# Performance work log

Measured on AMD Instinct MI355X. Metric: run time of the kernel, lower is better.

The kernel has to match this reference:

```python
import jax, jax.numpy as jnp
import numpy as np

N_NODES = 200000  # num_users + num_items
N_EDGES = 500000
LATENT = 64
N_LAYERS = 3
NEG_SLOPE = 0.01  # F.leaky_relu default
EPS = 1e-16       # PyG geo_softmax denominator epsilon


def setup_inputs() -> dict:
    key = jax.random.key(0)
    k1, k2, k3, k4, k5 = jax.random.split(key, 5)
    edge_index = jax.random.randint(k1, (2, N_EDGES), 0, N_NODES, dtype=jnp.int64 if jax.config.jax_enable_x64 else jnp.int32)
    edge_attrs = jax.random.normal(k2, (N_EDGES, 2), dtype=jnp.float32)
    emb = jax.random.normal(k3, (N_NODES, LATENT), dtype=jnp.float32)
    # per-layer attention params, shape [L, heads=1 -> squeezed, in_channels]
    a_att_w = jax.random.normal(k4, (N_LAYERS, LATENT), dtype=jnp.float32) * 0.1
    r_att_w = jax.random.normal(k5, (N_LAYERS, LATENT), dtype=jnp.float32) * 0.1
    return {"edge_index": edge_index, "edge_attrs": edge_attrs, "emb": emb,
            "a_att_w": a_att_w, "r_att_w": r_att_w}


def _segment_softmax(scores, dst, num_nodes):
    # scores: [E, D] softmax over edges grouped by destination node (PyG geo_softmax)
    m = jax.ops.segment_max(scores, dst, num_segments=num_nodes)  # [N, D]
    m = jnp.where(jnp.isfinite(m), m, 0.0)  # nodes without incoming edges
    w = jnp.exp(scores - m[dst])
    den = jax.ops.segment_sum(w, dst, num_segments=num_nodes)     # [N, D]
    return w / (den[dst] + EPS)


def reference(edge_index, edge_attrs, emb, a_att_w, r_att_w):
    src, dst = edge_index[0], edge_index[1]
    n = emb.shape[0]
    # symmetric degree normalization (degree of destination endpoints)
    deg = jax.ops.segment_sum(jnp.ones_like(dst, dtype=emb.dtype), dst, num_segments=n)
    dinv = jnp.where(deg > 0, deg ** -0.5, 0.0)
    norm = (dinv[src] * dinv[dst])[:, None]  # [E, 1]

    a_e = edge_attrs[:, 0:1]  # [E, 1]
    r_e = edge_attrs[:, 1:2]

    x = emb
    acc = emb  # layer-0 embedding
    for l in range(N_LAYERS):
        scores = (jax.nn.leaky_relu(a_e * a_att_w[l], NEG_SLOPE)
                  + jax.nn.leaky_relu(r_e * r_att_w[l], NEG_SLOPE))  # [E, D]
        attn = _segment_softmax(scores, dst, n)                       # [E, D]
        msg = norm * attn * x[src]                                    # gather + weight
        x = jax.ops.segment_sum(msg, dst, num_segments=n)             # scatter-add
        acc = acc + x
    out = acc / (N_LAYERS + 1)  # mean over layer embeddings
    return out
```

## Files before the change

kernel.cpp:

```cpp
#include <hip/hip_runtime.h>

#define BLK 256
#define LBLK 256
#define CH 1024

__device__ __forceinline__ unsigned short f2bf(float f) {
    unsigned u = __float_as_uint(f);
    u += 0x7FFFu + ((u >> 16) & 1u);
    return (unsigned short)(u >> 16);
}
__device__ __forceinline__ float bf2f(unsigned short h) {
    return __uint_as_float((unsigned)h << 16);
}
__device__ __forceinline__ float4 unpack4(ushort4 h) {
    return make_float4(bf2f(h.x), bf2f(h.y), bf2f(h.z), bf2f(h.w));
}
__device__ __forceinline__ ushort4 pack4(float4 f) {
    ushort4 h; h.x = f2bf(f.x); h.y = f2bf(f.y); h.z = f2bf(f.z); h.w = f2bf(f.w);
    return h;
}


__global__ void k_deg(const int* __restrict__ dst, int* __restrict__ deg,
                      int* __restrict__ rank, int E) {
    int e = blockIdx.x * blockDim.x + threadIdx.x;
    if (e < E) rank[e] = atomicAdd(&deg[dst[e]], 1);
}

__global__ void k_scan1(const int* __restrict__ deg, int* __restrict__ partials, int N) {
    __shared__ int sm[BLK];
    int i0 = blockIdx.x * CH + threadIdx.x * 4;
    int s = 0;
    if (i0 + 3 < N) {
        int4 v = *(const int4*)(deg + i0);
        s = (v.x + v.y) + (v.z + v.w);
    } else {
        for (int k = 0; k < 4; ++k) if (i0 + k < N) s += deg[i0 + k];
    }
    sm[threadIdx.x] = s;
    __syncthreads();
    for (int off = BLK / 2; off > 0; off >>= 1) {
        if (threadIdx.x < off) sm[threadIdx.x] += sm[threadIdx.x + off];
        __syncthreads();
    }
    if (threadIdx.x == 0) partials[blockIdx.x] = sm[0];
}

__global__ void k_scan2(const int* __restrict__ deg, const int* __restrict__ partials,
                        int* __restrict__ row_off, int N, int E, int nb) {
    __shared__ int sp[BLK];
    __shared__ int sm[BLK];
    int b = blockIdx.x, t = threadIdx.x;
    sp[t] = (t < nb) ? partials[t] : 0;
    __syncthreads();
    for (int off = 1; off < BLK; off <<= 1) {
        int add = (t >= off) ? sp[t - off] : 0;
        __syncthreads();
        sp[t] += add;
        __syncthreads();
    }
    int base = (b == 0) ? 0 : sp[b - 1];
    if (b == 0 && t == 0) row_off[N] = E;
    int i0 = b * CH + t * 4;
    int v0 = 0, v1 = 0, v2 = 0, v3 = 0;
    if (i0 + 3 < N) {
        int4 v = *(const int4*)(deg + i0);
        v0 = v.x; v1 = v.y; v2 = v.z; v3 = v.w;
    } else {
        if (i0     < N) v0 = deg[i0];
        if (i0 + 1 < N) v1 = deg[i0 + 1];
        if (i0 + 2 < N) v2 = deg[i0 + 2];
    }
    int tot = (v0 + v1) + (v2 + v3);
    sm[t] = tot;
    __syncthreads();
    for (int off = 1; off < BLK; off <<= 1) {
        int add = (t >= off) ? sm[t - off] : 0;
        __syncthreads();
        sm[t] += add;
        __syncthreads();
    }
    int excl = base + sm[t] - tot;
    int4 r;
    r.x = excl;
    r.y = excl + v0;
    r.z = excl + v0 + v1;
    r.w = excl + v0 + v1 + v2;
    if (i0 + 3 < N) {
        *(int4*)(row_off + i0) = r;
    } else {
        if (i0     < N) row_off[i0]     = r.x;
        if (i0 + 1 < N) row_off[i0 + 1] = r.y;
        if (i0 + 2 < N) row_off[i0 + 2] = r.z;
    }
}

__global__ void k_convfill(const int* __restrict__ src, const int* __restrict__ dst,
                           const float2* __restrict__ attrs, const int* __restrict__ row_off,
                           const int* __restrict__ rank, const int* __restrict__ deg,
                           uint2* __restrict__ csr, const float4* __restrict__ emb4,
                           ushort4* __restrict__ embs, int E, int N16, int gF) {
    int b = blockIdx.x;
    if (b < gF) {
        int e = b * BLK + threadIdx.x;
        if (e >= E) return;
        int pos = row_off[dst[e]] + rank[e];
        float2 ar = attrs[e];
        csr[pos] = make_uint2((unsigned)src[e],
                              (unsigned)f2bf(ar.x) | ((unsigned)f2bf(ar.y) << 16));
    } else {
        int i = (b - gF) * BLK + threadIdx.x;
        if (i >= N16) return;
        int d = deg[i >> 4];
        float dinv = (d > 0) ? rsqrtf((float)d) : 0.0f;
        float4 e = emb4[i];
        embs[i] = pack4(make_float4(dinv * e.x, dinv * e.y, dinv * e.z, dinv * e.w));
    }
}


__device__ __forceinline__ float lrelu(float x) { return fmaxf(x, 0.01f * x); }

__device__ __forceinline__ float4 edge_w4(unsigned ar, const float4& aw, const float4& rw) {
    float a = bf2f((unsigned short)(ar & 0xffffu));
    float r = bf2f((unsigned short)(ar >> 16));
    float4 w;
    w.x = __expf(lrelu(a * aw.x) + lrelu(r * rw.x));
    w.y = __expf(lrelu(a * aw.y) + lrelu(r * rw.y));
    w.z = __expf(lrelu(a * aw.z) + lrelu(r * rw.z));
    w.w = __expf(lrelu(a * aw.w) + lrelu(r * rw.w));
    return w;
}

__device__ __forceinline__ void acc4(float4& num, float4& den,
                                     const float4& w, const ushort4& h, float g) {
    float4 x = unpack4(h);
    den.x += g * w.x; den.y += g * w.y; den.z += g * w.z; den.w += g * w.w;
    num.x += g * w.x * x.x;
    num.y += g * w.y * x.y;
    num.z += g * w.z * x.z;
    num.w += g * w.w * x.w;
}

template<int MODE>
__global__ __launch_bounds__(LBLK) void k_layer(
    const ushort4* __restrict__ xs, const uint2* __restrict__ csr,
    const int* __restrict__ row_off,
    const float4* __restrict__ aw4, const float4* __restrict__ rw4,
    const float4* __restrict__ emb4,
    const ushort4* __restrict__ xsA, const ushort4* __restrict__ xsB,
    ushort4* __restrict__ xsout, float4* __restrict__ out4, int N) {
    const int t = threadIdx.x;
    const int d4 = t & 15;
    const int v = blockIdx.x * (LBLK / 16) + (t >> 4);
    if (v >= N) return;
    const float4 aw = aw4[d4];
    const float4 rw = rw4[d4];
    const int s0 = row_off[v];
    const int s1 = row_off[v + 1];
    const int dv = s1 - s0;
    float4 num = {0.f, 0.f, 0.f, 0.f};
    float4 den = {0.f, 0.f, 0.f, 0.f};
    for (int i = s0; i < s1; i += 4) {
        const int last = s1 - 1;
        uint2 e0 = csr[i];
        uint2 e1 = csr[min(i + 1, last)];
        uint2 e2 = csr[min(i + 2, last)];
        uint2 e3 = csr[min(i + 3, last)];
        ushort4 h0 = xs[(size_t)e0.x * 16 + d4];
        ushort4 h1 = xs[(size_t)e1.x * 16 + d4];
        ushort4 h2 = xs[(size_t)e2.x * 16 + d4];
        ushort4 h3 = xs[(size_t)e3.x * 16 + d4];
        float4 w0 = edge_w4(e0.y, aw, rw);
        float4 w1 = edge_w4(e1.y, aw, rw);
        float4 w2 = edge_w4(e2.y, aw, rw);
        float4 w3 = edge_w4(e3.y, aw, rw);
        float g1 = (i + 1 < s1) ? 1.0f : 0.0f;
        float g2 = (i + 2 < s1) ? 1.0f : 0.0f;
        float g3 = (i + 3 < s1) ? 1.0f : 0.0f;
        acc4(num, den, w0, h0, 1.0f);
        acc4(num, den, w1, h1, g1);
        acc4(num, den, w2, h2, g2);
        acc4(num, den, w3, h3, g3);
    }
    float4 xr;
    xr.x = num.x / (den.x + 1e-16f);
    xr.y = num.y / (den.y + 1e-16f);
    xr.z = num.z / (den.z + 1e-16f);
    xr.w = num.w / (den.w + 1e-16f);
    const float dinv = (dv > 0) ? rsqrtf((float)dv) : 0.0f;
    const size_t o = (size_t)v * 16 + d4;
    if (MODE == 2) {
        const float sd = (dv > 0) ? sqrtf((float)dv) : 0.0f;
        float4 e = emb4[o];
        float4 A = unpack4(xsA[o]);
        float4 B = unpack4(xsB[o]);
        float4 r;
        r.x = (e.x + sd * (A.x + B.x) + dinv * xr.x) * 0.25f;
        r.y = (e.y + sd * (A.y + B.y) + dinv * xr.y) * 0.25f;
        r.z = (e.z + sd * (A.z + B.z) + dinv * xr.z) * 0.25f;
        r.w = (e.w + sd * (A.w + B.w) + dinv * xr.w) * 0.25f;
        out4[o] = r;
    } else {
        const float s = dinv * dinv;
        xsout[o] = pack4(make_float4(s * xr.x, s * xr.y, s * xr.z, s * xr.w));
    }
}


extern "C" void kernel_launch(void* const* d_in, const int* in_sizes, int n_in,
                              void* d_out, int out_size, void* d_ws, size_t ws_size,
                              hipStream_t stream) {
    const int*   ei    = (const int*)d_in[0];
    const float* attrs = (const float*)d_in[1];
    const float* emb   = (const float*)d_in[2];
    const float* a_att = (const float*)d_in[3];
    const float* r_att = (const float*)d_in[4];

    const int E = in_sizes[0] / 2;
    const int N = in_sizes[2] / 64;
    const int* src = ei;
    const int* dst = ei + E;

    char* ws = (char*)d_ws;
    size_t off = 0;
    auto alloc = [&](size_t bytes) {
        void* p = ws + off;
        off += (bytes + 255) & ~(size_t)255;
        return p;
    };
    int*     deg      = (int*)alloc((size_t)N * 4);
    int*     rank     = (int*)alloc((size_t)E * 4);
    int*     row_off  = (int*)alloc((size_t)(N + 1) * 4);
    int*     partials = (int*)alloc((size_t)BLK * 4);
    uint2*   csr      = (uint2*)alloc((size_t)E * 8);
    ushort4* embs     = (ushort4*)alloc((size_t)N * 16 * 8);
    ushort4* xsA      = (ushort4*)alloc((size_t)N * 16 * 8);
    ushort4* xsB      = (ushort4*)alloc((size_t)N * 16 * 8);
    float4*  out      = (float4*)d_out;

    hipMemsetAsync(deg, 0, (size_t)N * 4, stream);

    int gE = (E + BLK - 1) / BLK;
    int nb = (N + CH - 1) / CH;
    int gF = gE;
    int gC = (N * 16 + BLK - 1) / BLK;

    k_deg     <<<gE, BLK, 0, stream>>>(dst, deg, rank, E);
    k_scan1   <<<nb, BLK, 0, stream>>>(deg, partials, N);
    k_scan2   <<<nb, BLK, 0, stream>>>(deg, partials, row_off, N, E, nb);
    k_convfill<<<gF + gC, BLK, 0, stream>>>(src, dst, (const float2*)attrs, row_off,
                                            rank, deg, csr, (const float4*)emb,
                                            embs, E, N * 16, gF);

    const float4* emb4 = (const float4*)emb;
    const float4* aw4  = (const float4*)a_att;
    const float4* rw4  = (const float4*)r_att;

    int gL = (N + (LBLK / 16) - 1) / (LBLK / 16);
    k_layer<0><<<gL, LBLK, 0, stream>>>(embs, csr, row_off, aw4,      rw4,
                                        nullptr, nullptr, nullptr, xsA, nullptr, N);
    k_layer<1><<<gL, LBLK, 0, stream>>>(xsA,  csr, row_off, aw4 + 16, rw4 + 16,
                                        nullptr, nullptr, nullptr, xsB, nullptr, N);
    k_layer<2><<<gL, LBLK, 0, stream>>>(xsB,  csr, row_off, aw4 + 32, rw4 + 32,
                                        emb4, xsA, xsB, nullptr, out, N);
}
```

Before: 242.2 us.

## Fuse two-pass scan into one kernel with inter-block flags; use exp2 weights

Replaces the two scan kernels with one. Each block publishes its flagged partial sum with a release store, then spin-waits on all earlier partials through acquire loads before computing its prefix. This removes one kernel launch and its dependency gap, but it only works if all 196 blocks run at the same time. Separately, the edge-weight exponent uses exp2f with the attention weights pre-scaled by log2(e), and tail edges are masked by a large negative bias inside the exponent instead of multiplying by a gate.

```diff
diff --git a/kernel.cpp b/kernel.cpp
--- a/kernel.cpp
+++ b/kernel.cpp
@@ -3,6 +3,8 @@
 #define BLK 256
 #define LBLK 256
 #define CH 1024
+#define LOG2E 1.44269504f
+#define SFLAG 0x40000000
 
 __device__ __forceinline__ unsigned short f2bf(float f) {
     unsigned u = __float_as_uint(f);
@@ -27,40 +29,11 @@
     if (e < E) rank[e] = atomicAdd(&deg[dst[e]], 1);
 }
 
-__global__ void k_scan1(const int* __restrict__ deg, int* __restrict__ partials, int N) {
+__global__ void k_scan(const int* __restrict__ deg, int* __restrict__ sync,
+                       int* __restrict__ row_off, int N, int E, int nb) {
     __shared__ int sm[BLK];
-    int i0 = blockIdx.x * CH + threadIdx.x * 4;
-    int s = 0;
-    if (i0 + 3 < N) {
-        int4 v = *(const int4*)(deg + i0);
-        s = (v.x + v.y) + (v.z + v.w);
-    } else {
-        for (int k = 0; k < 4; ++k) if (i0 + k < N) s += deg[i0 + k];
-    }
-    sm[threadIdx.x] = s;
-    __syncthreads();
-    for (int off = BLK / 2; off > 0; off >>= 1) {
-        if (threadIdx.x < off) sm[threadIdx.x] += sm[threadIdx.x + off];
-        __syncthreads();
-    }
-    if (threadIdx.x == 0) partials[blockIdx.x] = sm[0];
-}
-
-__global__ void k_scan2(const int* __restrict__ deg, const int* __restrict__ partials,
-                        int* __restrict__ row_off, int N, int E, int nb) {
     __shared__ int sp[BLK];
-    __shared__ int sm[BLK];
     int b = blockIdx.x, t = threadIdx.x;
-    sp[t] = (t < nb) ? partials[t] : 0;
-    __syncthreads();
-    for (int off = 1; off < BLK; off <<= 1) {
-        int add = (t >= off) ? sp[t - off] : 0;
-        __syncthreads();
-        sp[t] += add;
-        __syncthreads();
-    }
-    int base = (b == 0) ? 0 : sp[b - 1];
-    if (b == 0 && t == 0) row_off[N] = E;
     int i0 = b * CH + t * 4;
     int v0 = 0, v1 = 0, v2 = 0, v3 = 0;
     if (i0 + 3 < N) {
@@ -80,6 +53,25 @@
         sm[t] += add;
         __syncthreads();
     }
+    if (t == 0)
+        __hip_atomic_store(&sync[b], sm[BLK - 1] | SFLAG,
+                           __ATOMIC_RELEASE, __HIP_MEMORY_SCOPE_AGENT);
+    int pv = 0;
+    if (t < nb) {
+        while ((pv = __hip_atomic_load(&sync[t], __ATOMIC_ACQUIRE,
+                                       __HIP_MEMORY_SCOPE_AGENT)) == 0) {}
+        pv &= ~SFLAG;
+    }
+    sp[t] = pv;
+    __syncthreads();
+    for (int off = 1; off < BLK; off <<= 1) {
+        int add = (t >= off) ? sp[t - off] : 0;
+        __syncthreads();
+        sp[t] += add;
+        __syncthreads();
+    }
+    int base = (b == 0) ? 0 : sp[b - 1];
+    if (b == 0 && t == 0) row_off[N] = E;
     int excl = base + sm[t] - tot;
     int4 r;
     r.x = excl;
@@ -121,25 +113,26 @@
 
 __device__ __forceinline__ float lrelu(float x) { return fmaxf(x, 0.01f * x); }
 
-__device__ __forceinline__ float4 edge_w4(unsigned ar, const float4& aw, const float4& rw) {
+__device__ __forceinline__ float4 edge_w4(unsigned ar, const float4& aw, const float4& rw,
+                                          float gb) {
     float a = bf2f((unsigned short)(ar & 0xffffu));
     float r = bf2f((unsigned short)(ar >> 16));
     float4 w;
-    w.x = __expf(lrelu(a * aw.x) + lrelu(r * rw.x));
-    w.y = __expf(lrelu(a * aw.y) + lrelu(r * rw.y));
-    w.z = __expf(lrelu(a * aw.z) + lrelu(r * rw.z));
-    w.w = __expf(lrelu(a * aw.w) + lrelu(r * rw.w));
+    w.x = exp2f(lrelu(a * aw.x) + lrelu(r * rw.x) + gb);
+    w.y = exp2f(lrelu(a * aw.y) + lrelu(r * rw.y) + gb);
+    w.z = exp2f(lrelu(a * aw.z) + lrelu(r * rw.z) + gb);
+    w.w = exp2f(lrelu(a * aw.w) + lrelu(r * rw.w) + gb);
     return w;
 }
 
 __device__ __forceinline__ void acc4(float4& num, float4& den,
-                                     const float4& w, const ushort4& h, float g) {
+                                     const float4& w, const ushort4& h) {
     float4 x = unpack4(h);
-    den.x += g * w.x; den.y += g * w.y; den.z += g * w.z; den.w += g * w.w;
-    num.x += g * w.x * x.x;
-    num.y += g * w.y * x.y;
-    num.z += g * w.z * x.z;
-    num.w += g * w.w * x.w;
+    den.x += w.x; den.y += w.y; den.z += w.z; den.w += w.w;
+    num.x += w.x * x.x;
+    num.y += w.y * x.y;
+    num.z += w.z * x.z;
+    num.w += w.w * x.w;
 }
 
 template<int MODE>
@@ -154,8 +147,10 @@
     const int d4 = t & 15;
     const int v = blockIdx.x * (LBLK / 16) + (t >> 4);
     if (v >= N) return;
-    const float4 aw = aw4[d4];
-    const float4 rw = rw4[d4];
+    float4 aw = aw4[d4];
+    float4 rw = rw4[d4];
+    aw.x *= LOG2E; aw.y *= LOG2E; aw.z *= LOG2E; aw.w *= LOG2E;
+    rw.x *= LOG2E; rw.y *= LOG2E; rw.z *= LOG2E; rw.w *= LOG2E;
     const int s0 = row_off[v];
     const int s1 = row_off[v + 1];
     const int dv = s1 - s0;
@@ -171,17 +166,17 @@
         ushort4 h1 = xs[(size_t)e1.x * 16 + d4];
         ushort4 h2 = xs[(size_t)e2.x * 16 + d4];
         ushort4 h3 = xs[(size_t)e3.x * 16 + d4];
-        float4 w0 = edge_w4(e0.y, aw, rw);
-        float4 w1 = edge_w4(e1.y, aw, rw);
-        float4 w2 = edge_w4(e2.y, aw, rw);
-        float4 w3 = edge_w4(e3.y, aw, rw);
-        float g1 = (i + 1 < s1) ? 1.0f : 0.0f;
-        float g2 = (i + 2 < s1) ? 1.0f : 0.0f;
-        float g3 = (i + 3 < s1) ? 1.0f : 0.0f;
-        acc4(num, den, w0, h0, 1.0f);
-        acc4(num, den, w1, h1, g1);
-        acc4(num, den, w2, h2, g2);
-        acc4(num, den, w3, h3, g3);
+        float gb1 = (i + 1 < s1) ? 0.0f : -1e4f;
+        float gb2 = (i + 2 < s1) ? 0.0f : -1e4f;
+        float gb3 = (i + 3 < s1) ? 0.0f : -1e4f;
+        float4 w0 = edge_w4(e0.y, aw, rw, 0.0f);
+        float4 w1 = edge_w4(e1.y, aw, rw, gb1);
+        float4 w2 = edge_w4(e2.y, aw, rw, gb2);
+        float4 w3 = edge_w4(e3.y, aw, rw, gb3);
+        acc4(num, den, w0, h0);
+        acc4(num, den, w1, h1);
+        acc4(num, den, w2, h2);
+        acc4(num, den, w3, h3);
     }
     float4 xr;
     xr.x = num.x / (den.x + 1e-16f);
@@ -230,16 +225,16 @@
         return p;
     };
     int*     deg      = (int*)alloc((size_t)N * 4);
+    int*     sync     = (int*)alloc((size_t)BLK * 4);
     int*     rank     = (int*)alloc((size_t)E * 4);
     int*     row_off  = (int*)alloc((size_t)(N + 1) * 4);
-    int*     partials = (int*)alloc((size_t)BLK * 4);
     uint2*   csr      = (uint2*)alloc((size_t)E * 8);
     ushort4* embs     = (ushort4*)alloc((size_t)N * 16 * 8);
     ushort4* xsA      = (ushort4*)alloc((size_t)N * 16 * 8);
     ushort4* xsB      = (ushort4*)alloc((size_t)N * 16 * 8);
     float4*  out      = (float4*)d_out;
 
-    hipMemsetAsync(deg, 0, (size_t)N * 4, stream);
+    hipMemsetAsync(deg, 0, (size_t)N * 4 + (size_t)BLK * 4, stream);
 
     int gE = (E + BLK - 1) / BLK;
     int nb = (N + CH - 1) / CH;
@@ -247,8 +242,7 @@
     int gC = (N * 16 + BLK - 1) / BLK;
 
     k_deg     <<<gE, BLK, 0, stream>>>(dst, deg, rank, E);
-    k_scan1   <<<nb, BLK, 0, stream>>>(deg, partials, N);
-    k_scan2   <<<nb, BLK, 0, stream>>>(deg, partials, row_off, N, E, nb);
+    k_scan    <<<nb, BLK, 0, stream>>>(deg, sync, row_off, N, E, nb);
     k_convfill<<<gF + gC, BLK, 0, stream>>>(src, dst, (const float2*)attrs, row_off,
                                             rank, deg, csr, (const float4*)emb,
                                             embs, E, N * 16, gF);
```

Result: slower. 276.7 us (+14.2%).
